# Optimization experiments

Hardware: AMD Instinct MI355X
Metric: run time of the kernel (lower is better)

The kernel has to match this reference:

```python
import jax, jax.numpy as jnp
import numpy as np


def setup_inputs() -> dict:
    key = jax.random.key(0)
    k1, k2, k3, k4 = jax.random.split(key, 4)
    B, Cin, Cout, H, W = 8, 256, 256, 128, 128
    x = jax.random.normal(k1, (B, Cin, H, W), dtype=jnp.float32)
    delta_weight = jax.random.normal(k2, (B, Cout, Cin, 1, 1), dtype=jnp.float32) * 0.02
    dw_weight = jax.random.normal(k3, (Cin, 1, 3, 3), dtype=jnp.float32) * 0.05
    pw_weight = jax.random.normal(k4, (Cout, Cin, 1, 1), dtype=jnp.float32) * 0.05
    return {"x": x, "delta_weight": delta_weight, "dw_weight": dw_weight, "pw_weight": pw_weight}


def reference(x, delta_weight, dw_weight, pw_weight):
    # Depthwise 3x3 conv, padding=1, groups=Cin. Kernel OIHW = (Cin, 1, 3, 3).
    Cin = x.shape[1]
    out = jax.lax.conv_general_dilated(
        x, dw_weight,
        window_strides=(1, 1), padding=((1, 1), (1, 1)),
        dimension_numbers=("NCHW", "OIHW", "NCHW"),
        feature_group_count=Cin,
    )
    # Per-sample pointwise 1x1: w_final[b] = pw_weight + delta_weight[b]; batched GEMM.
    w_final = pw_weight[None, :, :, 0, 0] + delta_weight[:, :, :, 0, 0]  # (B, Cout, Cin)
    out = jnp.einsum("bchw,boc->bohw", out, w_final)
    return out
```

## Files before the change

kernel.cpp:

```cpp
#include <hip/hip_runtime.h>

#define BATCH 8
#define CIN   256
#define COUT  256
#define HH    128
#define WW    128
#define HW    (HH*WW)

typedef __bf16 bf16x8 __attribute__((ext_vector_type(8)));
typedef float  f32x4  __attribute__((ext_vector_type(4)));

__device__ __forceinline__ unsigned short f2bf(float f) {
    unsigned u = __float_as_uint(f);
    unsigned r = (u + 0x7fffu + ((u >> 16) & 1u)) >> 16;
    return (unsigned short)r;
}

__global__ __launch_bounds__(256) void prep_w_kernel(
    const float* __restrict__ delta, const float* __restrict__ pw,
    unsigned short* __restrict__ Wb)
{
    int i = blockIdx.x * 256 + threadIdx.x;
    float4 d = *(const float4*)(delta + (size_t)i * 4);
    int j = (i * 4) & (COUT * CIN - 1);
    float4 p = *(const float4*)(pw + j);
    ushort4 r;
    r.x = f2bf(d.x + p.x);
    r.y = f2bf(d.y + p.y);
    r.z = f2bf(d.z + p.z);
    r.w = f2bf(d.w + p.w);
    *(ushort4*)(Wb + (size_t)i * 4) = r;
}

__global__ __launch_bounds__(256) void dwconv_kernel(
    const float* __restrict__ x, const float* __restrict__ dw,
    unsigned short* __restrict__ Tt)
{
    __shared__ unsigned short tile[128 * 66];
    __shared__ float kw[64 * 9];

    const int h  = blockIdx.x;
    const int cb = blockIdx.y;
    const int b  = blockIdx.z;
    const int tid = threadIdx.x;

    if (tid < 144) {
        float4 v = *(const float4*)(dw + (size_t)cb * 576 + (size_t)tid * 4);
        *(float4*)(kw + tid * 4) = v;
    }
    __syncthreads();

    const int wq = tid & 31;
    const int cs = tid >> 5;
    const int w0 = wq * 4;

    for (int ci = 0; ci < 8; ++ci) {
        const int c = ci * 8 + cs;
        const float* xp = x + ((size_t)(b * CIN + cb * 64 + c)) * HW;
        const float* kc = kw + c * 9;
        float a0 = 0.f, a1 = 0.f, a2 = 0.f, a3 = 0.f;
        #pragma unroll
        for (int dy = 0; dy < 3; ++dy) {
            const int r = h + dy - 1;
            float4 v = {0.f, 0.f, 0.f, 0.f};
            if (r >= 0 && r < HH) v = *(const float4*)(xp + r * WW + w0);
            float lft = __shfl_up(v.w, 1);
            float rgt = __shfl_down(v.x, 1);
            if (wq == 0)  lft = 0.f;
            if (wq == 31) rgt = 0.f;
            const float k0 = kc[dy * 3 + 0], k1 = kc[dy * 3 + 1], k2 = kc[dy * 3 + 2];
            a0 += k0 * lft + k1 * v.x + k2 * v.y;
            a1 += k0 * v.x + k1 * v.y + k2 * v.z;
            a2 += k0 * v.y + k1 * v.z + k2 * v.w;
            a3 += k0 * v.z + k1 * v.w + k2 * rgt;
        }
        const int base = w0 * 66 + c;
        tile[base]       = f2bf(a0);
        tile[base + 66]  = f2bf(a1);
        tile[base + 132] = f2bf(a2);
        tile[base + 198] = f2bf(a3);
    }
    __syncthreads();

    {
        const int cpair = tid & 31;
        const int wg    = tid >> 5;
        const size_t prow = (size_t)b * HW + (size_t)h * WW;
        #pragma unroll
        for (int wi = 0; wi < 16; ++wi) {
            const int w = wg * 16 + wi;
            unsigned v = *(const unsigned*)&tile[w * 66 + cpair * 2];
            *(unsigned*)&Tt[(prow + w) * CIN + cb * 64 + cpair * 2] = v;
        }
    }
}

__global__ __launch_bounds__(256) void gemm_kernel(
    const unsigned short* __restrict__ Wb,
    const unsigned short* __restrict__ Tt,
    float* __restrict__ out)
{
    __shared__ unsigned short lA[128 * 32];
    __shared__ unsigned short lB[128 * 32];

    const int nt = blockIdx.x;
    const int mt = blockIdx.y;
    const int b  = blockIdx.z;
    const int tid = threadIdx.x;

    const unsigned short* Ab = Wb + ((size_t)b * COUT + mt * 128) * CIN;
    const unsigned short* Bb = Tt + ((size_t)b * HW + nt * 128) * CIN;

    const int lane = tid & 63;
    const int wv   = tid >> 6;
    const int wm   = (wv & 1) * 64;
    const int wn   = (wv >> 1) * 64;
    const int q    = lane >> 4;
    const int rrow = lane & 15;

    const int arow = tid >> 2;
    const int acol = (tid & 3) * 8;

    f32x4 acc[4][4] = {};

    for (int k0 = 0; k0 < CIN; k0 += 32) {
        #pragma unroll
        for (int r = 0; r < 2; ++r) {
            const int row = r * 64 + arow;
            const unsigned short* ga = Ab + (size_t)row * CIN + k0 + acol;
            const unsigned short* gb = Bb + (size_t)row * CIN + k0 + acol;
            __builtin_amdgcn_global_load_lds(
                (const __attribute__((address_space(1))) void*)ga,
                (__attribute__((address_space(3))) void*)(lA + (size_t)(r * 256 + tid) * 8),
                16, 0, 0);
            __builtin_amdgcn_global_load_lds(
                (const __attribute__((address_space(1))) void*)gb,
                (__attribute__((address_space(3))) void*)(lB + (size_t)(r * 256 + tid) * 8),
                16, 0, 0);
        }
        __syncthreads();

        bf16x8 af[4], bfv[4];
        #pragma unroll
        for (int i = 0; i < 4; ++i) {
            af[i]  = *(const bf16x8*)&lA[(wm + i * 16 + rrow) * 32 + q * 8];
            bfv[i] = *(const bf16x8*)&lB[(wn + i * 16 + rrow) * 32 + q * 8];
        }
        #pragma unroll
        for (int i = 0; i < 4; ++i)
            #pragma unroll
            for (int j = 0; j < 4; ++j)
                acc[i][j] = __builtin_amdgcn_mfma_f32_16x16x32_bf16(af[i], bfv[j], acc[i][j], 0, 0, 0);
        __syncthreads();
    }

    float* outp = out + ((size_t)b * COUT + mt * 128 + wm) * HW + (size_t)nt * 128 + wn;
    #pragma unroll
    for (int i = 0; i < 4; ++i)
        #pragma unroll
        for (int j = 0; j < 4; ++j)
            #pragma unroll
            for (int rr = 0; rr < 4; ++rr)
                outp[(size_t)(i * 16 + q * 4 + rr) * HW + j * 16 + rrow] = acc[i][j][rr];
}

extern "C" void kernel_launch(void* const* d_in, const int* in_sizes, int n_in,
                              void* d_out, int out_size, void* d_ws, size_t ws_size,
                              hipStream_t stream)
{
    const float* x     = (const float*)d_in[0];
    const float* delta = (const float*)d_in[1];
    const float* dw    = (const float*)d_in[2];
    const float* pw    = (const float*)d_in[3];
    float* out = (float*)d_out;

    unsigned short* Tt = (unsigned short*)d_ws;
    unsigned short* Wb = (unsigned short*)((char*)d_ws + (size_t)BATCH * HW * CIN * 2);

    prep_w_kernel<<<dim3(512), dim3(256), 0, stream>>>(delta, pw, Wb);
    dwconv_kernel<<<dim3(128, 4, 8), dim3(256), 0, stream>>>(x, dw, Tt);
    gemm_kernel<<<dim3(128, 2, 8), dim3(256), 0, stream>>>(Wb, Tt, out);
}
```

Baseline: 286.5 us.

## Fuse weight prep, depthwise conv and pointwise GEMM into one kernel

Replaces the three-kernel pipeline with a single kernel that computes per-sample bf16 weights and the depthwise 3x3 conv directly into swizzled LDS tiles, then runs MFMA on them. This removes the global round trip of the bf16 intermediate and the separate weight buffer, plus two launches. In exchange each row block recomputes the conv for both output-channel halves, re-reading x, and recomputes the weight conversion per tile. K-chunk size grows to 64 with an XOR swizzle to avoid LDS bank conflicts.

```diff
diff --git a/kernel.cpp b/kernel.cpp
--- a/kernel.cpp
+++ b/kernel.cpp
@@ -9,6 +9,7 @@
 
 typedef __bf16 bf16x8 __attribute__((ext_vector_type(8)));
 typedef float  f32x4  __attribute__((ext_vector_type(4)));
+typedef unsigned short u16x8 __attribute__((ext_vector_type(8)));
 
 __device__ __forceinline__ unsigned short f2bf(float f) {
     unsigned u = __float_as_uint(f);
@@ -16,100 +17,21 @@
     return (unsigned short)r;
 }
 
-__global__ __launch_bounds__(256) void prep_w_kernel(
+__device__ __forceinline__ int swz8(int r) { return (r ^ (r >> 2)) & 7; }
+
+__global__ __launch_bounds__(256, 4) void fused_kernel(
+    const float* __restrict__ x, const float* __restrict__ dw,
     const float* __restrict__ delta, const float* __restrict__ pw,
-    unsigned short* __restrict__ Wb)
-{
-    int i = blockIdx.x * 256 + threadIdx.x;
-    float4 d = *(const float4*)(delta + (size_t)i * 4);
-    int j = (i * 4) & (COUT * CIN - 1);
-    float4 p = *(const float4*)(pw + j);
-    ushort4 r;
-    r.x = f2bf(d.x + p.x);
-    r.y = f2bf(d.y + p.y);
-    r.z = f2bf(d.z + p.z);
-    r.w = f2bf(d.w + p.w);
-    *(ushort4*)(Wb + (size_t)i * 4) = r;
-}
-
-__global__ __launch_bounds__(256) void dwconv_kernel(
-    const float* __restrict__ x, const float* __restrict__ dw,
-    unsigned short* __restrict__ Tt)
-{
-    __shared__ unsigned short tile[128 * 66];
-    __shared__ float kw[64 * 9];
-
-    const int h  = blockIdx.x;
-    const int cb = blockIdx.y;
-    const int b  = blockIdx.z;
-    const int tid = threadIdx.x;
-
-    if (tid < 144) {
-        float4 v = *(const float4*)(dw + (size_t)cb * 576 + (size_t)tid * 4);
-        *(float4*)(kw + tid * 4) = v;
-    }
-    __syncthreads();
-
-    const int wq = tid & 31;
-    const int cs = tid >> 5;
-    const int w0 = wq * 4;
-
-    for (int ci = 0; ci < 8; ++ci) {
-        const int c = ci * 8 + cs;
-        const float* xp = x + ((size_t)(b * CIN + cb * 64 + c)) * HW;
-        const float* kc = kw + c * 9;
-        float a0 = 0.f, a1 = 0.f, a2 = 0.f, a3 = 0.f;
-        #pragma unroll
-        for (int dy = 0; dy < 3; ++dy) {
-            const int r = h + dy - 1;
-            float4 v = {0.f, 0.f, 0.f, 0.f};
-            if (r >= 0 && r < HH) v = *(const float4*)(xp + r * WW + w0);
-            float lft = __shfl_up(v.w, 1);
-            float rgt = __shfl_down(v.x, 1);
-            if (wq == 0)  lft = 0.f;
-            if (wq == 31) rgt = 0.f;
-            const float k0 = kc[dy * 3 + 0], k1 = kc[dy * 3 + 1], k2 = kc[dy * 3 + 2];
-            a0 += k0 * lft + k1 * v.x + k2 * v.y;
-            a1 += k0 * v.x + k1 * v.y + k2 * v.z;
-            a2 += k0 * v.y + k1 * v.z + k2 * v.w;
-            a3 += k0 * v.z + k1 * v.w + k2 * rgt;
-        }
-        const int base = w0 * 66 + c;
-        tile[base]       = f2bf(a0);
-        tile[base + 66]  = f2bf(a1);
-        tile[base + 132] = f2bf(a2);
-        tile[base + 198] = f2bf(a3);
-    }
-    __syncthreads();
-
-    {
-        const int cpair = tid & 31;
-        const int wg    = tid >> 5;
-        const size_t prow = (size_t)b * HW + (size_t)h * WW;
-        #pragma unroll
-        for (int wi = 0; wi < 16; ++wi) {
-            const int w = wg * 16 + wi;
-            unsigned v = *(const unsigned*)&tile[w * 66 + cpair * 2];
-            *(unsigned*)&Tt[(prow + w) * CIN + cb * 64 + cpair * 2] = v;
-        }
-    }
-}
-
-__global__ __launch_bounds__(256) void gemm_kernel(
-    const unsigned short* __restrict__ Wb,
-    const unsigned short* __restrict__ Tt,
     float* __restrict__ out)
 {
-    __shared__ unsigned short lA[128 * 32];
-    __shared__ unsigned short lB[128 * 32];
+    __shared__ unsigned short lA[128 * 64];
+    __shared__ unsigned short lB[128 * 64];
 
-    const int nt = blockIdx.x;
-    const int mt = blockIdx.y;
-    const int b  = blockIdx.z;
-    const int tid = threadIdx.x;
-
-    const unsigned short* Ab = Wb + ((size_t)b * COUT + mt * 128) * CIN;
-    const unsigned short* Bb = Tt + ((size_t)b * HW + nt * 128) * CIN;
+    const int b     = (int)blockIdx.x & 7;
+    const int inner = (int)blockIdx.x >> 3;
+    const int mt    = inner & 1;
+    const int h     = inner >> 1;
+    const int tid   = threadIdx.x;
 
     const int lane = tid & 63;
     const int wv   = tid >> 6;
@@ -118,43 +40,85 @@
     const int q    = lane >> 4;
     const int rrow = lane & 15;
 
-    const int arow = tid >> 2;
-    const int acol = (tid & 3) * 8;
+    const int wq = tid & 31;
+    const int cs = tid >> 5;
+    const int w0 = wq * 4;
 
     f32x4 acc[4][4] = {};
 
-    for (int k0 = 0; k0 < CIN; k0 += 32) {
+    const float* deltab = delta + (size_t)b * COUT * CIN;
+
+    for (int kc = 0; kc < 4; ++kc) {
         #pragma unroll
-        for (int r = 0; r < 2; ++r) {
-            const int row = r * 64 + arow;
-            const unsigned short* ga = Ab + (size_t)row * CIN + k0 + acol;
-            const unsigned short* gb = Bb + (size_t)row * CIN + k0 + acol;
-            __builtin_amdgcn_global_load_lds(
-                (const __attribute__((address_space(1))) void*)ga,
-                (__attribute__((address_space(3))) void*)(lA + (size_t)(r * 256 + tid) * 8),
-                16, 0, 0);
-            __builtin_amdgcn_global_load_lds(
-                (const __attribute__((address_space(1))) void*)gb,
-                (__attribute__((address_space(3))) void*)(lB + (size_t)(r * 256 + tid) * 8),
-                16, 0, 0);
+        for (int r = 0; r < 4; ++r) {
+            const int i   = r * 256 + tid;
+            const int row = i >> 3;
+            const int ls  = i & 7;
+            const size_t goff = (size_t)(mt * 128 + row) * CIN + kc * 64 + ls * 8;
+            const float4 p0 = *(const float4*)(pw + goff);
+            const float4 p1 = *(const float4*)(pw + goff + 4);
+            const float4 d0 = *(const float4*)(deltab + goff);
+            const float4 d1 = *(const float4*)(deltab + goff + 4);
+            u16x8 v;
+            v[0] = f2bf(p0.x + d0.x); v[1] = f2bf(p0.y + d0.y);
+            v[2] = f2bf(p0.z + d0.z); v[3] = f2bf(p0.w + d0.w);
+            v[4] = f2bf(p1.x + d1.x); v[5] = f2bf(p1.y + d1.y);
+            v[6] = f2bf(p1.z + d1.z); v[7] = f2bf(p1.w + d1.w);
+            *(u16x8*)&lA[row * 64 + (ls ^ swz8(row)) * 8] = v;
         }
+
+        u16x8 v0, v1, v2, v3;
+        #pragma unroll
+        for (int ci = 0; ci < 8; ++ci) {
+            const int gc = kc * 64 + cs * 8 + ci;
+            const float* xp = x + ((size_t)(b * CIN + gc)) * HW;
+            const float* kp = dw + (size_t)gc * 9;
+            float a0 = 0.f, a1 = 0.f, a2 = 0.f, a3 = 0.f;
+            #pragma unroll
+            for (int dy = 0; dy < 3; ++dy) {
+                const int r = h + dy - 1;
+                float4 v = {0.f, 0.f, 0.f, 0.f};
+                if (r >= 0 && r < HH) v = *(const float4*)(xp + r * WW + w0);
+                float lft = __shfl_up(v.w, 1);
+                float rgt = __shfl_down(v.x, 1);
+                if (wq == 0)  lft = 0.f;
+                if (wq == 31) rgt = 0.f;
+                const float k0 = kp[dy * 3 + 0], k1 = kp[dy * 3 + 1], k2 = kp[dy * 3 + 2];
+                a0 += k0 * lft + k1 * v.x + k2 * v.y;
+                a1 += k0 * v.x + k1 * v.y + k2 * v.z;
+                a2 += k0 * v.y + k1 * v.z + k2 * v.w;
+                a3 += k0 * v.z + k1 * v.w + k2 * rgt;
+            }
+            v0[ci] = f2bf(a0); v1[ci] = f2bf(a1);
+            v2[ci] = f2bf(a2); v3[ci] = f2bf(a3);
+        }
+        *(u16x8*)&lB[(w0 + 0) * 64 + (cs ^ swz8(w0 + 0)) * 8] = v0;
+        *(u16x8*)&lB[(w0 + 1) * 64 + (cs ^ swz8(w0 + 1)) * 8] = v1;
+        *(u16x8*)&lB[(w0 + 2) * 64 + (cs ^ swz8(w0 + 2)) * 8] = v2;
+        *(u16x8*)&lB[(w0 + 3) * 64 + (cs ^ swz8(w0 + 3)) * 8] = v3;
+
         __syncthreads();
 
-        bf16x8 af[4], bfv[4];
         #pragma unroll
-        for (int i = 0; i < 4; ++i) {
-            af[i]  = *(const bf16x8*)&lA[(wm + i * 16 + rrow) * 32 + q * 8];
-            bfv[i] = *(const bf16x8*)&lB[(wn + i * 16 + rrow) * 32 + q * 8];
+        for (int kk = 0; kk < 2; ++kk) {
+            bf16x8 af[4], bfv[4];
+            #pragma unroll
+            for (int i = 0; i < 4; ++i) {
+                const int ra = wm + i * 16 + rrow;
+                const int rb = wn + i * 16 + rrow;
+                af[i]  = *(const bf16x8*)&lA[ra * 64 + ((kk * 4 + q) ^ swz8(ra)) * 8];
+                bfv[i] = *(const bf16x8*)&lB[rb * 64 + ((kk * 4 + q) ^ swz8(rb)) * 8];
+            }
+            #pragma unroll
+            for (int i = 0; i < 4; ++i)
+                #pragma unroll
+                for (int j = 0; j < 4; ++j)
+                    acc[i][j] = __builtin_amdgcn_mfma_f32_16x16x32_bf16(af[i], bfv[j], acc[i][j], 0, 0, 0);
         }
-        #pragma unroll
-        for (int i = 0; i < 4; ++i)
-            #pragma unroll
-            for (int j = 0; j < 4; ++j)
-                acc[i][j] = __builtin_amdgcn_mfma_f32_16x16x32_bf16(af[i], bfv[j], acc[i][j], 0, 0, 0);
         __syncthreads();
     }
 
-    float* outp = out + ((size_t)b * COUT + mt * 128 + wm) * HW + (size_t)nt * 128 + wn;
+    float* outp = out + ((size_t)(b * COUT + mt * 128 + wm)) * HW + (size_t)h * WW + wn;
     #pragma unroll
     for (int i = 0; i < 4; ++i)
         #pragma unroll
@@ -174,10 +138,5 @@
     const float* pw    = (const float*)d_in[3];
     float* out = (float*)d_out;
 
-    unsigned short* Tt = (unsigned short*)d_ws;
-    unsigned short* Wb = (unsigned short*)((char*)d_ws + (size_t)BATCH * HW * CIN * 2);
-
-    prep_w_kernel<<<dim3(512), dim3(256), 0, stream>>>(delta, pw, Wb);
-    dwconv_kernel<<<dim3(128, 4, 8), dim3(256), 0, stream>>>(x, dw, Tt);
-    gemm_kernel<<<dim3(128, 2, 8), dim3(256), 0, stream>>>(Wb, Tt, out);
+    fused_kernel<<<dim3(2048), dim3(256), 0, stream>>>(x, dw, delta, pw, out);
 }
```

New measurement: 1.052 ms. 267% more time.
